# Performance work log

Hardware: AMD Instinct MI355X
Metric: run time of the kernel (lower is better)

## Reference

```python
import jax, jax.numpy as jnp
import numpy as np

D = 2048
MAX_SEQ_LEN = 8192
LN_EPS = 1e-5


def _spine(max_len):
    s = [0, 2, 4]
    while True:
        nv = 2 * (s[-1] + s[-2] + s[-3])
        if nv >= max_len:
            break
        s.append(nv)
    return s


def setup_inputs() -> dict:
    key = jax.random.key(0)
    k0, k1 = jax.random.split(key, 2)
    B, S = 8, 8192
    x = jax.random.normal(k0, (B, S, D), dtype=jnp.float32)
    # LearnedHarmonicBasis params (torch init values)
    ones = jnp.ones((D,), jnp.float32)
    zeros = jnp.zeros((D,), jnp.float32)
    return {
        "x": x,
        "alpha_xz": ones, "beta_xy": -ones, "gamma_x": zeros,
        "alpha_wy": ones, "beta_wx": -ones, "gamma_w": zeros,
        "alpha_xv": ones, "beta_wv": -ones, "gamma_v": zeros,
        # nn.Linear(2D, D): weight [D, 2D], bias [D]
        "gate_w": (jax.random.normal(k1, (D, 2 * D), jnp.float32) / np.float32(np.sqrt(2 * D))),
        "gate_b": zeros,
        "ln_w": ones,
        "ln_b": zeros,
    }


def _layernorm(v, w, b):
    m = jnp.mean(v, axis=-1, keepdims=True)
    var = jnp.var(v, axis=-1, keepdims=True)
    return (v - m) * jax.lax.rsqrt(var + LN_EPS) * w + b


def reference(x, alpha_xz, beta_xy, gamma_x, alpha_wy, beta_wx, gamma_w,
              alpha_xv, beta_wv, gamma_v, gate_w, gate_b, ln_w, ln_b):
    S = x.shape[1]
    rel = [i for i in _spine(MAX_SEQ_LEN) if i < S]  # static at trace time
    h = x
    for k in range(3, len(rel)):  # strictly sequential spine recurrence
        pz, py, px = rel[k], rel[k - 1], rel[k - 2]
        z = h[:, pz, :]        # (B, D)
        y = h[:, py, :]
        x_prev = h[:, px, :]
        x_new = alpha_xz * z + beta_xy * y + gamma_x
        w = alpha_wy * y + beta_wx * x_prev + gamma_w
        v = alpha_xv * x_new + beta_wv * w + gamma_v
        # HierarchicalInjectionGate(v, z)
        g = jax.nn.sigmoid(jnp.concatenate([v, z], axis=-1) @ gate_w.T + gate_b)
        v_inj = _layernorm(g * v + (1.0 - g) * z, ln_w, ln_b)
        h = h.at[:, pz, :].set(v_inj)
    return h
```

## Files before the change

kernel.cpp:

```cpp
#include <hip/hip_runtime.h>

#define DD 2048
#define SS 8192
#define BB 8
#define TWO_D 4096
#define LN_EPS 1e-5f
#define NCHAIN 256
#define SLICE  9364
#define NCOPY  1171
#define TOTROWS (BB * SS)

typedef float f32x4 __attribute__((ext_vector_type(4)));
typedef unsigned short u16;
typedef u16 u16x8 __attribute__((ext_vector_type(8)));

__device__ __forceinline__ bool is_spine(int r) {
    return (r==12)|(r==36)|(r==104)|(r==304)|(r==888)|(r==2592)|(r==7568);
}

__device__ __forceinline__ float bf2f(u16 h) {
    union { unsigned u; float f; } c; c.u = ((unsigned)h) << 16; return c.f;
}

__global__ __launch_bounds__(256) void cvtw(
    const float* __restrict__ gw, u16* __restrict__ gwb)
{
    const int i = (blockIdx.x * 256 + threadIdx.x) * 8;
    const f32x4 a = __builtin_nontemporal_load((const f32x4*)(gw + i));
    const f32x4 b = __builtin_nontemporal_load((const f32x4*)(gw + i + 4));
    const float v[8] = {a.x, a.y, a.z, a.w, b.x, b.y, b.z, b.w};
    u16x8 o;
#pragma unroll
    for (int k = 0; k < 8; ++k) {
        union { float f; unsigned u; } c; c.f = v[k];
        o[k] = (u16)((c.u + 0x7FFFu + ((c.u >> 16) & 1u)) >> 16);
    }
    *(u16x8*)(gwb + i) = o;
}

template<int WBF>
__global__ __launch_bounds__(256) void k1t(
    const float* __restrict__ x, int pz, long long crbase,
    const float* __restrict__ ybase, unsigned long long ybstr,
    const float* __restrict__ pbase, unsigned long long pbstr,
    const float* __restrict__ a_xz, const float* __restrict__ b_xy, const float* __restrict__ g_x,
    const float* __restrict__ a_wy, const float* __restrict__ b_wx, const float* __restrict__ g_w,
    const float* __restrict__ a_xv, const float* __restrict__ b_wv, const float* __restrict__ g_v,
    const void* __restrict__ gwv, const float* __restrict__ gate_b,
    float* __restrict__ u_out, float* __restrict__ out)
{
    __shared__ float lds[BB][DD];
    const int tid = threadIdx.x, lane = tid & 63, wave = tid >> 6;
    const size_t bstr_x = (size_t)SS * DD;

    if (blockIdx.x >= NCHAIN) {
        const int cb = blockIdx.x - NCHAIN;
        const long long rbase = crbase + (long long)cb * 8;
        const f32x4* src4 = (const f32x4*)x;
        f32x4* dst4 = (f32x4*)out;
        for (int rr = wave; rr < 8; rr += 4) {
            const long long row = rbase + rr;
            if (row >= (long long)TOTROWS) continue;
            if (is_spine((int)(row & (SS - 1)))) continue;
            const f32x4* s = src4 + (size_t)row * 512;
            f32x4*       d = dst4 + (size_t)row * 512;
#pragma unroll
            for (int k = 0; k < 8; ++k) {
                const f32x4 v = __builtin_nontemporal_load(&s[lane + 64 * k]);
                __builtin_nontemporal_store(v, &d[lane + 64 * k]);
            }
        }
        return;
    }

    const float* zrow = x + (size_t)pz * DD;

    for (int dd = 0; dd < DD; dd += 256) {
        const int d = dd + tid;
        const float axz = a_xz[d], bxy = b_xy[d], gx  = g_x[d];
        const float awy = a_wy[d], bwx = b_wx[d], gww = g_w[d];
        const float axv = a_xv[d], bwv = b_wv[d], gv  = g_v[d];
#pragma unroll
        for (int b = 0; b < BB; ++b) {
            const float z  = zrow[(size_t)b * bstr_x + d];
            const float y  = ybase[(size_t)b * ybstr + d];
            const float xp = pbase[(size_t)b * pbstr + d];
            lds[b][d] = axv * (axz * z + bxy * y + gx)
                      + bwv * (awy * y + bwx * xp + gww) + gv;
        }
    }
    __syncthreads();

    const int d0 = blockIdx.x * 8 + wave * 2;
    const int myb = lane & 7, myc = (lane >> 3) & 1;

    float a0[8], a1[8];
#pragma unroll
    for (int b = 0; b < 8; ++b) { a0[b] = 0.f; a1[b] = 0.f; }

    if constexpr (WBF) {
        const u16* gw0 = (const u16*)gwv + (size_t)d0 * TWO_D;
        const u16* gw1 = gw0 + TWO_D;
        for (int j = lane * 8; j < DD; j += 512) {
            const u16x8 w0 = *(const u16x8*)(gw0 + j);
            const u16x8 w1 = *(const u16x8*)(gw1 + j);
            float wf0[8], wf1[8];
#pragma unroll
            for (int k = 0; k < 8; ++k) { wf0[k] = bf2f(w0[k]); wf1[k] = bf2f(w1[k]); }
#pragma unroll
            for (int b = 0; b < 8; ++b) {
                const f32x4 v0 = *(const f32x4*)&lds[b][j];
                const f32x4 v1 = *(const f32x4*)&lds[b][j + 4];
                a0[b] += wf0[0]*v0.x + wf0[1]*v0.y + wf0[2]*v0.z + wf0[3]*v0.w
                       + wf0[4]*v1.x + wf0[5]*v1.y + wf0[6]*v1.z + wf0[7]*v1.w;
                a1[b] += wf1[0]*v0.x + wf1[1]*v0.y + wf1[2]*v0.z + wf1[3]*v0.w
                       + wf1[4]*v1.x + wf1[5]*v1.y + wf1[6]*v1.z + wf1[7]*v1.w;
            }
        }
    } else {
        const float* gw0 = (const float*)gwv + (size_t)d0 * TWO_D;
        const float* gw1 = gw0 + TWO_D;
        for (int j = lane * 4; j < DD; j += 256) {
            const float4 w0 = *(const float4*)(gw0 + j);
            const float4 w1 = *(const float4*)(gw1 + j);
#pragma unroll
            for (int b = 0; b < 8; ++b) {
                const float4 vv = *(const float4*)&lds[b][j];
                a0[b] += w0.x*vv.x + w0.y*vv.y + w0.z*vv.z + w0.w*vv.w;
                a1[b] += w1.x*vv.x + w1.y*vv.y + w1.z*vv.z + w1.w*vv.w;
            }
        }
    }
    const float vmine = (lane < 16) ? lds[myb][d0 + myc] : 0.f;
    __syncthreads();

    for (int d4 = tid; d4 < 512; d4 += 256) {
#pragma unroll
        for (int b = 0; b < BB; ++b)
            ((f32x4*)&lds[b][0])[d4] = ((const f32x4*)(zrow + (size_t)b * bstr_x))[d4];
    }
    __syncthreads();

    if constexpr (WBF) {
        const u16* gw0 = (const u16*)gwv + (size_t)d0 * TWO_D + DD;
        const u16* gw1 = gw0 + TWO_D;
        for (int j = lane * 8; j < DD; j += 512) {
            const u16x8 w0 = *(const u16x8*)(gw0 + j);
            const u16x8 w1 = *(const u16x8*)(gw1 + j);
            float wf0[8], wf1[8];
#pragma unroll
            for (int k = 0; k < 8; ++k) { wf0[k] = bf2f(w0[k]); wf1[k] = bf2f(w1[k]); }
#pragma unroll
            for (int b = 0; b < 8; ++b) {
                const f32x4 v0 = *(const f32x4*)&lds[b][j];
                const f32x4 v1 = *(const f32x4*)&lds[b][j + 4];
                a0[b] += wf0[0]*v0.x + wf0[1]*v0.y + wf0[2]*v0.z + wf0[3]*v0.w
                       + wf0[4]*v1.x + wf0[5]*v1.y + wf0[6]*v1.z + wf0[7]*v1.w;
                a1[b] += wf1[0]*v0.x + wf1[1]*v0.y + wf1[2]*v0.z + wf1[3]*v0.w
                       + wf1[4]*v1.x + wf1[5]*v1.y + wf1[6]*v1.z + wf1[7]*v1.w;
            }
        }
    } else {
        const float* gw0 = (const float*)gwv + (size_t)d0 * TWO_D + DD;
        const float* gw1 = gw0 + TWO_D;
        for (int j = lane * 4; j < DD; j += 256) {
            const float4 w0 = *(const float4*)(gw0 + j);
            const float4 w1 = *(const float4*)(gw1 + j);
#pragma unroll
            for (int b = 0; b < 8; ++b) {
                const float4 zz = *(const float4*)&lds[b][j];
                a0[b] += w0.x*zz.x + w0.y*zz.y + w0.z*zz.z + w0.w*zz.w;
                a1[b] += w1.x*zz.x + w1.y*zz.y + w1.z*zz.z + w1.w*zz.w;
            }
        }
    }
#pragma unroll
    for (int b = 0; b < 8; ++b) {
#pragma unroll
        for (int off = 32; off >= 1; off >>= 1) {
            a0[b] += __shfl_xor(a0[b], off);
            a1[b] += __shfl_xor(a1[b], off);
        }
    }
    if (lane < 16) {
        const int d = d0 + myc;
        const float tot = myc ? a1[myb] : a0[myb];
        const float zmv = lds[myb][d];
        const float gg  = 1.f / (1.f + __expf(-(tot + gate_b[d])));
        u_out[myb * DD + d] = gg * vmine + (1.f - gg) * zmv;
    }
}

__global__ __launch_bounds__(256) void k2_ln(
    const float* __restrict__ u, const float* __restrict__ lnw,
    const float* __restrict__ lnb, float* __restrict__ dst,
    float* __restrict__ out, int pz)
{
    const int b = blockIdx.x, tid = threadIdx.x;
    const float* ub = u + b * DD;
    float vals[8];
    float s = 0.f, sq = 0.f;
#pragma unroll
    for (int i = 0; i < 8; ++i) {
        const float t = ub[tid + 256 * i];
        vals[i] = t; s += t; sq += t * t;
    }
    const int wave = tid >> 6, lane = tid & 63;
#pragma unroll
    for (int off = 32; off >= 1; off >>= 1) {
        s  += __shfl_xor(s, off);
        sq += __shfl_xor(sq, off);
    }
    __shared__ float red[2][4];
    if (lane == 0) { red[0][wave] = s; red[1][wave] = sq; }
    __syncthreads();
    s  = red[0][0] + red[0][1] + red[0][2] + red[0][3];
    sq = red[1][0] + red[1][1] + red[1][2] + red[1][3];
    const float mean = s * (1.f / DD);
    const float var  = sq * (1.f / DD) - mean * mean;
    const float rs   = rsqrtf(var + LN_EPS);
    float* db = dst + b * DD;
    float* ob = out + (size_t)b * SS * DD + (size_t)pz * DD;
#pragma unroll
    for (int i = 0; i < 8; ++i) {
        const int d = tid + 256 * i;
        const float r = (vals[i] - mean) * rs * lnw[d] + lnb[d];
        db[d] = r;
        ob[d] = r;
    }
}

extern "C" void kernel_launch(void* const* d_in, const int* in_sizes, int n_in,
                              void* d_out, int out_size, void* d_ws, size_t ws_size,
                              hipStream_t stream)
{
    const float* x      = (const float*)d_in[0];
    const float* a_xz   = (const float*)d_in[1];
    const float* b_xy   = (const float*)d_in[2];
    const float* g_x    = (const float*)d_in[3];
    const float* a_wy   = (const float*)d_in[4];
    const float* b_wx   = (const float*)d_in[5];
    const float* g_w    = (const float*)d_in[6];
    const float* a_xv   = (const float*)d_in[7];
    const float* b_wv   = (const float*)d_in[8];
    const float* g_v    = (const float*)d_in[9];
    const float* gate_w = (const float*)d_in[10];
    const float* gate_b = (const float*)d_in[11];
    const float* ln_w   = (const float*)d_in[12];
    const float* ln_b   = (const float*)d_in[13];
    float* out = (float*)d_out;

    float* u_buf = (float*)d_ws;
    float* res   = u_buf + BB * DD;
    const size_t head = (size_t)(BB * DD + 7 * BB * DD) * 4;
    u16* gwb = (u16*)((char*)d_ws + head);
    const size_t need = head + (size_t)DD * TWO_D * 2;
    const bool usebf = (ws_size >= need);

    static const int PZ[7] = {12, 36, 104, 304, 888, 2592, 7568};
    static const int PY[7] = {4, 12, 36, 104, 304, 888, 2592};
    static const int PX[7] = {2, 4, 12, 36, 104, 304, 888};

    if (usebf)
        hipLaunchKernelGGL(cvtw, dim3((DD * TWO_D) / (256 * 8)), dim3(256), 0, stream,
                           gate_w, gwb);

    long long c1 = 0;
    for (int it = 0; it < 7; ++it) {
        const float* ybase; unsigned long long ybstr;
        const float* pbase; unsigned long long pbstr;
        if (it == 0) { ybase = x + (size_t)PY[0] * DD; ybstr = (size_t)SS * DD; }
        else         { ybase = res + (size_t)(it - 1) * BB * DD; ybstr = DD; }
        if (it <= 1) { pbase = x + (size_t)PX[it] * DD; pbstr = (size_t)SS * DD; }
        else         { pbase = res + (size_t)(it - 2) * BB * DD; pbstr = DD; }

        if (usebf)
            hipLaunchKernelGGL((k1t<1>), dim3(NCHAIN + NCOPY), dim3(256), 0, stream,
                               x, PZ[it], c1, ybase, ybstr, pbase, pbstr,
                               a_xz, b_xy, g_x, a_wy, b_wx, g_w, a_xv, b_wv, g_v,
                               (const void*)gwb, gate_b, u_buf, out);
        else
            hipLaunchKernelGGL((k1t<0>), dim3(NCHAIN + NCOPY), dim3(256), 0, stream,
                               x, PZ[it], c1, ybase, ybstr, pbase, pbstr,
                               a_xz, b_xy, g_x, a_wy, b_wx, g_w, a_xv, b_wv, g_v,
                               (const void*)gate_w, gate_b, u_buf, out);
        c1 += SLICE;

        hipLaunchKernelGGL(k2_ln, dim3(BB), dim3(256), 0, stream,
                           u_buf, ln_w, ln_b, res + (size_t)it * BB * DD,
                           out, PZ[it]);
    }
}
```

Measured before the change: 256.2 us.

## Split bulk row copy across gate and layernorm kernels to overlap with LN

The non-spine row copy that was overlapped only with the gate GEMV kernel is now divided between it and the layernorm kernel. The LN kernel gains extra copy blocks so it no longer runs on just 8 blocks while the GPU idles. The aim is to hide more of the large memory copy behind both sequential stages. The per-kernel slice sizes are fixed constants (7*6800 + 7*2565 covers the 65536 rows), and the split may steal bandwidth from the LN critical path.

```diff
diff --git a/kernel.cpp b/kernel.cpp
--- a/kernel.cpp
+++ b/kernel.cpp
@@ -6,8 +6,10 @@
 #define TWO_D 4096
 #define LN_EPS 1e-5f
 #define NCHAIN 256
-#define SLICE  9364
-#define NCOPY  1171
+#define S1     6800
+#define NCOPY1 850
+#define S2     2565
+#define NCOPY2 321
 #define TOTROWS (BB * SS)
 
 typedef float f32x4 __attribute__((ext_vector_type(4)));
@@ -20,6 +22,26 @@
 
 __device__ __forceinline__ float bf2f(u16 h) {
     union { unsigned u; float f; } c; c.u = ((unsigned)h) << 16; return c.f;
+}
+
+__device__ __forceinline__ void copy_rows_nt(
+    const float* __restrict__ x, float* __restrict__ out,
+    long long rbase, long long rend, int lane, int wave)
+{
+    const f32x4* src4 = (const f32x4*)x;
+    f32x4* dst4 = (f32x4*)out;
+    for (int rr = wave; rr < 8; rr += 4) {
+        const long long row = rbase + rr;
+        if (row >= rend || row >= (long long)TOTROWS) continue;
+        if (is_spine((int)(row & (SS - 1)))) continue;
+        const f32x4* s = src4 + (size_t)row * 512;
+        f32x4*       d = dst4 + (size_t)row * 512;
+#pragma unroll
+        for (int k = 0; k < 8; ++k) {
+            const f32x4 v = __builtin_nontemporal_load(&s[lane + 64 * k]);
+            __builtin_nontemporal_store(v, &d[lane + 64 * k]);
+        }
+    }
 }
 
 __global__ __launch_bounds__(256) void cvtw(
@@ -55,21 +77,7 @@
 
     if (blockIdx.x >= NCHAIN) {
         const int cb = blockIdx.x - NCHAIN;
-        const long long rbase = crbase + (long long)cb * 8;
-        const f32x4* src4 = (const f32x4*)x;
-        f32x4* dst4 = (f32x4*)out;
-        for (int rr = wave; rr < 8; rr += 4) {
-            const long long row = rbase + rr;
-            if (row >= (long long)TOTROWS) continue;
-            if (is_spine((int)(row & (SS - 1)))) continue;
-            const f32x4* s = src4 + (size_t)row * 512;
-            f32x4*       d = dst4 + (size_t)row * 512;
-#pragma unroll
-            for (int k = 0; k < 8; ++k) {
-                const f32x4 v = __builtin_nontemporal_load(&s[lane + 64 * k]);
-                __builtin_nontemporal_store(v, &d[lane + 64 * k]);
-            }
-        }
+        copy_rows_nt(x, out, crbase + (long long)cb * 8, crbase + S1, lane, wave);
         return;
     }
 
@@ -191,12 +199,21 @@
     }
 }
 
-__global__ __launch_bounds__(256) void k2_ln(
+__global__ __launch_bounds__(256) void k2f(
+    const float* __restrict__ x, long long crbase,
     const float* __restrict__ u, const float* __restrict__ lnw,
     const float* __restrict__ lnb, float* __restrict__ dst,
     float* __restrict__ out, int pz)
 {
-    const int b = blockIdx.x, tid = threadIdx.x;
+    const int tid = threadIdx.x, lane = tid & 63, wave = tid >> 6;
+
+    if (blockIdx.x >= 8) {
+        const int cb = blockIdx.x - 8;
+        copy_rows_nt(x, out, crbase + (long long)cb * 8, crbase + S2, lane, wave);
+        return;
+    }
+
+    const int b = blockIdx.x;
     const float* ub = u + b * DD;
     float vals[8];
     float s = 0.f, sq = 0.f;
@@ -205,7 +222,6 @@
         const float t = ub[tid + 256 * i];
         vals[i] = t; s += t; sq += t * t;
     }
-    const int wave = tid >> 6, lane = tid & 63;
 #pragma unroll
     for (int off = 32; off >= 1; off >>= 1) {
         s  += __shfl_xor(s, off);
@@ -265,7 +281,8 @@
         hipLaunchKernelGGL(cvtw, dim3((DD * TWO_D) / (256 * 8)), dim3(256), 0, stream,
                            gate_w, gwb);
 
-    long long c1 = 0;
+    long long c1 = 0, c2 = (long long)7 * S1;
+
     for (int it = 0; it < 7; ++it) {
         const float* ybase; unsigned long long ybstr;
         const float* pbase; unsigned long long pbstr;
@@ -275,19 +292,20 @@
         else         { pbase = res + (size_t)(it - 2) * BB * DD; pbstr = DD; }
 
         if (usebf)
-            hipLaunchKernelGGL((k1t<1>), dim3(NCHAIN + NCOPY), dim3(256), 0, stream,
+            hipLaunchKernelGGL((k1t<1>), dim3(NCHAIN + NCOPY1), dim3(256), 0, stream,
                                x, PZ[it], c1, ybase, ybstr, pbase, pbstr,
                                a_xz, b_xy, g_x, a_wy, b_wx, g_w, a_xv, b_wv, g_v,
                                (const void*)gwb, gate_b, u_buf, out);
         else
-            hipLaunchKernelGGL((k1t<0>), dim3(NCHAIN + NCOPY), dim3(256), 0, stream,
+            hipLaunchKernelGGL((k1t<0>), dim3(NCHAIN + NCOPY1), dim3(256), 0, stream,
                                x, PZ[it], c1, ybase, ybstr, pbase, pbstr,
                                a_xz, b_xy, g_x, a_wy, b_wx, g_w, a_xv, b_wv, g_v,
                                (const void*)gate_w, gate_b, u_buf, out);
-        c1 += SLICE;
-
-        hipLaunchKernelGGL(k2_ln, dim3(BB), dim3(256), 0, stream,
-                           u_buf, ln_w, ln_b, res + (size_t)it * BB * DD,
-                           out, PZ[it]);
-    }
-}
+        c1 += S1;
+
+        hipLaunchKernelGGL(k2f, dim3(8 + NCOPY2), dim3(256), 0, stream,
+                           x, c2, u_buf, ln_w, ln_b,
+                           res + (size_t)it * BB * DD, out, PZ[it]);
+        c2 += S2;
+    }
+}
```

Measured after the change: 286.8 us. 12.0% more time.
